# Kernel optimization log

Hardware: AMD Instinct MI355X
Metric: run time of the kernel (lower is better)

## Reference

```python
import jax, jax.numpy as jnp
import numpy as np

N_HEAD = 16
N_KV_HEAD = 8
HEAD_DIM = 128
N_EMBED = 2048
EPS = 1.1920929e-07  # torch default eps for fp32 rms_norm


def _apply_rotary_emb(x, cos, sin):
    # x: (B, T, H, D); cos/sin: (1, T, 1, D//2)  (nanochat-style half rotation)
    d = x.shape[-1] // 2
    x1, x2 = x[..., :d], x[..., d:]
    y1 = x1 * cos + x2 * sin
    y2 = -x1 * sin + x2 * cos
    return jnp.concatenate([y1, y2], axis=-1).astype(x.dtype)


def _rms_norm(x):
    return x * jax.lax.rsqrt(jnp.mean(jnp.square(x), axis=-1, keepdims=True) + EPS)


def setup_inputs() -> dict:
    key = jax.random.key(0)
    ks = jax.random.split(key, 5)
    B, T = 2, 2048
    kv_dim = N_KV_HEAD * HEAD_DIM
    x = jax.random.normal(ks[0], (B, T, N_EMBED), dtype=jnp.float32)
    w_attn = jax.random.normal(ks[1], (N_EMBED + 2 * kv_dim, N_EMBED), dtype=jnp.float32) * 0.02
    w_proj = jax.random.normal(ks[2], (N_EMBED, N_EMBED), dtype=jnp.float32) * 0.02
    # realistic RoPE tables
    half = HEAD_DIM // 2
    inv_freq = 1.0 / (10000.0 ** (jnp.arange(half, dtype=jnp.float32) / half))
    freqs = jnp.arange(T, dtype=jnp.float32)[:, None] * inv_freq[None, :]  # (T, half)
    cos = jnp.cos(freqs)[None, :, None, :]
    sin = jnp.sin(freqs)[None, :, None, :]
    return {"x": x, "w_attn": w_attn, "w_proj": w_proj, "cos": cos, "sin": sin}


def reference(x, w_attn, w_proj, cos, sin):
    B, T, C = x.shape
    kv_dim = N_KV_HEAD * HEAD_DIM
    qkv = jnp.einsum('btc,oc->bto', x, w_attn)  # (B, T, C + 2*kv_dim)
    q = qkv[..., :C].reshape(B, T, N_HEAD, HEAD_DIM)
    k = qkv[..., C:C + kv_dim].reshape(B, T, N_KV_HEAD, HEAD_DIM)
    v = qkv[..., C + kv_dim:].reshape(B, T, N_KV_HEAD, HEAD_DIM)
    q = _rms_norm(_apply_rotary_emb(q, cos, sin))
    k = _rms_norm(_apply_rotary_emb(k, cos, sin))
    # GQA: repeat kv heads to match query heads
    rep = N_HEAD // N_KV_HEAD
    k = jnp.repeat(k, rep, axis=2)  # (B, T, n_head, D)
    v = jnp.repeat(v, rep, axis=2)
    scale = 1.0 / jnp.sqrt(jnp.float32(HEAD_DIM))
    scores = jnp.einsum('bqhd,bkhd->bhqk', q, k) * scale  # (B, H, T, T)
    causal = jnp.tril(jnp.ones((T, T), dtype=bool))
    scores = jnp.where(causal[None, None], scores, jnp.finfo(scores.dtype).min)
    attn = jax.nn.softmax(scores, axis=-1)
    y = jnp.einsum('bhqk,bkhd->bqhd', attn, v).reshape(B, T, C)
    return jnp.einsum('btc,oc->bto', y, w_proj)
```

## Files before the change

### kernel.cpp

```cpp
#include <hip/hip_runtime.h>

#define B_ 2
#define T_ 2048
#define NH 16
#define NKV 8
#define HD 128
#define C_ 2048
#define KVD (NKV*HD)
#define QKVD (C_ + 2*KVD)
#define NTOK (B_*T_)

typedef __bf16 bf16_t;
typedef __bf16 bf16x2_t __attribute__((ext_vector_type(2)));
typedef __bf16 bf16x4_t __attribute__((ext_vector_type(4)));
typedef __bf16 bf16x8_t __attribute__((ext_vector_type(8)));
typedef float f32x4_t __attribute__((ext_vector_type(4)));
typedef float f32x16_t __attribute__((ext_vector_type(16)));
typedef int i32x4_t __attribute__((ext_vector_type(4)));

__device__ __forceinline__ f32x4_t mfma16(bf16x8_t a, bf16x8_t b, f32x4_t c) {
  return __builtin_amdgcn_mfma_f32_16x16x32_bf16(a, b, c, 0, 0, 0);
}
__device__ __forceinline__ f32x16_t mfma32(bf16x8_t a, bf16x8_t b, f32x16_t c) {
  return __builtin_amdgcn_mfma_f32_32x32x16_bf16(a, b, c, 0, 0, 0);
}
__device__ __forceinline__ f32x16_t zero16() {
  f32x16_t z;
  #pragma unroll
  for (int i = 0; i < 16; i++) z[i] = 0.f;
  return z;
}
__device__ __forceinline__ int pk2(float a, float b) {
  bf16x2_t t; t[0] = (bf16_t)a; t[1] = (bf16_t)b;
  return __builtin_bit_cast(int, t);
}

#define GLDS16(gp, lp) __builtin_amdgcn_global_load_lds( \
    (const __attribute__((address_space(1))) void*)(gp), \
    (__attribute__((address_space(3))) void*)(lp), 16, 0, 0)

#define CFENCE() asm volatile("" ::: "memory")

#define KSTR 132
#define VSTR 68

__global__ __launch_bounds__(256) void cvt3_kernel(const float* __restrict__ s0, bf16_t* __restrict__ d0,
                                                   const float* __restrict__ s1, bf16_t* __restrict__ d1,
                                                   const float* __restrict__ s2, bf16_t* __restrict__ d2) {
  int bid = blockIdx.x;
  const float* s; bf16_t* d; int off;
  if (bid < 8192)       { s = s0; d = d0; off = bid; }
  else if (bid < 16384) { s = s1; d = d1; off = bid - 8192; }
  else                  { s = s2; d = d2; off = bid - 16384; }
  int i = (off * 256 + threadIdx.x) * 4;
  const float4 v = *(const float4*)(s + i);
  bf16x4_t o;
  o[0] = (bf16_t)v.x; o[1] = (bf16_t)v.y; o[2] = (bf16_t)v.z; o[3] = (bf16_t)v.w;
  *(bf16x4_t*)(d + i) = o;
}

__global__ __launch_bounds__(512, 1) void gemm8p(const bf16_t* __restrict__ A,
                                                 const bf16_t* __restrict__ Bm,
                                                 bf16_t* __restrict__ Cb,
                                                 int M, int N, int K) {
  __shared__ __align__(16) bf16_t As[2][256 * 64];
  __shared__ __align__(16) bf16_t Bs[2][256 * 64];
  int tid = threadIdx.x;
  int wave = tid >> 6, lane = tid & 63;
  int quad = lane >> 4, l16 = lane & 15;
  int wm = wave >> 2, wn = wave & 3;
  int gx = gridDim.x, nwg = gx * gridDim.y;
  int flat = blockIdx.y * gx + blockIdx.x;
  int swz = (flat & 7) * (nwg >> 3) + (flat >> 3);
  int bm = (swz / gx) * 256, bn = (swz % gx) * 256;
  int scol = ((tid & 7) ^ ((tid >> 3) & 7)) * 8;
  int srow = tid >> 3;
  const bf16_t* pa = A + (size_t)(bm + srow) * K + scol;
  const bf16_t* pb = Bm + (size_t)(bn + srow) * K + scol;

#define STAGE_A8(buf, tile, h) { \
    GLDS16(pa + (size_t)((h)*128 + 0) * K + (size_t)(tile)*64, &As[buf][((h)*128 + 0 + wave*8)*64]); \
    GLDS16(pa + (size_t)((h)*128 + 64) * K + (size_t)(tile)*64, &As[buf][((h)*128 + 64 + wave*8)*64]); }
#define STAGE_B8(buf, tile, h) { \
    GLDS16(pb + (size_t)((h)*128 + 0) * K + (size_t)(tile)*64, &Bs[buf][((h)*128 + 0 + wave*8)*64]); \
    GLDS16(pb + (size_t)((h)*128 + 64) * K + (size_t)(tile)*64, &Bs[buf][((h)*128 + 64 + wave*8)*64]); }

  f32x4_t acc[8][4];
  #pragma unroll
  for (int i = 0; i < 8; i++)
    #pragma unroll
    for (int j = 0; j < 4; j++) acc[i][j] = (f32x4_t){0.f, 0.f, 0.f, 0.f};

  int nt = K >> 6;
  STAGE_A8(0, 0, 0); STAGE_A8(0, 0, 1); STAGE_B8(0, 0, 0); STAGE_B8(0, 0, 1);
  STAGE_B8(1, 1, 0); STAGE_B8(1, 1, 1);
  asm volatile("s_waitcnt vmcnt(4)" ::: "memory");
  CFENCE(); __builtin_amdgcn_s_barrier(); CFENCE();

  for (int s = 0; s < nt; ++s) {
    int b = s & 1;
    bf16x8_t bfr[4][2];
    #pragma unroll
    for (int jph = 0; jph < 4; ++jph) {
      const int kh = jph >> 1;
      const int mg = jph & 1;
      if (mg == 0) {
        #pragma unroll
        for (int ni = 0; ni < 4; ni++)
          bfr[ni][kh] = *(const bf16x8_t*)&Bs[b][(wn*64 + ni*16 + l16)*64 + (((kh*4 + quad) ^ (l16 & 7))*8)];
      }
      bf16x8_t af[4];
      #pragma unroll
      for (int i = 0; i < 4; i++)
        af[i] = *(const bf16x8_t*)&As[b][(wm*128 + (mg*4 + i)*16 + l16)*64 + (((kh*4 + quad) ^ (l16 & 7))*8)];
      if (jph == 0) { if (s + 1 < nt) STAGE_A8(1 - b, s + 1, 0); }
      if (jph == 1) { if (s + 1 < nt) STAGE_A8(1 - b, s + 1, 1); }
      if (jph == 3) {
        if (s + 2 < nt) {
          STAGE_B8(b, s + 2, 0);
          STAGE_B8(b, s + 2, 1);
          asm volatile("s_waitcnt vmcnt(4)" ::: "memory");
        } else {
          asm volatile("s_waitcnt vmcnt(0)" ::: "memory");
        }
      }
      CFENCE(); __builtin_amdgcn_s_barrier(); CFENCE();
      __builtin_amdgcn_s_setprio(1);
      #pragma unroll
      for (int i = 0; i < 4; i++)
        #pragma unroll
        for (int ni = 0; ni < 4; ni++)
          acc[mg*4 + i][ni] = mfma16(af[i], bfr[ni][kh], acc[mg*4 + i][ni]);
      __builtin_amdgcn_s_setprio(0);
      CFENCE(); __builtin_amdgcn_s_barrier(); CFENCE();
    }
  }
  #pragma unroll
  for (int mi = 0; mi < 8; mi++)
    #pragma unroll
    for (int ni = 0; ni < 4; ni++) {
      int row0 = bm + wm*128 + mi*16 + quad*4;
      int col  = bn + wn*64 + ni*16 + l16;
      #pragma unroll
      for (int r = 0; r < 4; r++)
        Cb[(size_t)(row0 + r) * N + col] = (bf16_t)acc[mi][ni][r];
    }
#undef STAGE_A8
#undef STAGE_B8
}

template<int BM>
__global__ __launch_bounds__(512, 1) void gemm_nt2(const bf16_t* __restrict__ A,
                                                   const bf16_t* __restrict__ Bm,
                                                   float* __restrict__ Cf, bf16_t* __restrict__ Cb,
                                                   int M, int N, int K) {
  constexpr int MR = BM / 32;
  constexpr int RA = BM / 64;
  __shared__ __align__(16) bf16_t As[2][BM * 64];
  __shared__ __align__(16) bf16_t Bs[2][256 * 64];
  int tid = threadIdx.x;
  int wave = tid >> 6, lane = tid & 63;
  int quad = lane >> 4, l16 = lane & 15;
  int wm = wave >> 2, wn = wave & 3;
  int gx = gridDim.x;
  int nwg = gx * gridDim.y;
  int flat = blockIdx.y * gx + blockIdx.x;
  int swz = (flat & 7) * (nwg >> 3) + (flat >> 3);
  int bm = (swz / gx) * BM, bn = (swz % gx) * 256;
  int scol = (((tid & 7) ^ ((tid >> 3) & 7))) * 8;
  const bf16_t* pa = A + (size_t)(bm + (tid >> 3)) * K + scol;
  const bf16_t* pb = Bm + (size_t)(bn + (tid >> 3)) * K + scol;

  f32x4_t acc[MR][4];
  #pragma unroll
  for (int i = 0; i < MR; i++)
    #pragma unroll
    for (int j = 0; j < 4; j++) acc[i][j] = (f32x4_t){0.f, 0.f, 0.f, 0.f};

  int nt = K >> 6;
  #pragma unroll
  for (int r = 0; r < RA; r++) GLDS16(pa + (size_t)(r * 64) * K, &As[0][(r * 64 + wave * 8) * 64]);
  #pragma unroll
  for (int r = 0; r < 4; r++)  GLDS16(pb + (size_t)(r * 64) * K, &Bs[0][(r * 64 + wave * 8) * 64]);
  __syncthreads();

  for (int t = 0; t < nt; t++) {
    int cur = t & 1;
    if (t + 1 < nt) {
      int k1 = (t + 1) * 64;
      #pragma unroll
      for (int r = 0; r < RA; r++) GLDS16(pa + (size_t)(r * 64) * K + k1, &As[1 - cur][(r * 64 + wave * 8) * 64]);
      #pragma unroll
      for (int r = 0; r < 4; r++)  GLDS16(pb + (size_t)(r * 64) * K + k1, &Bs[1 - cur][(r * 64 + wave * 8) * 64]);
    }
    bf16x8_t bfr[4][2];
    #pragma unroll
    for (int ni = 0; ni < 4; ni++)
      #pragma unroll
      for (int kh = 0; kh < 2; kh++) {
        int blk = (kh * 4 + quad) ^ (l16 & 7);
        bfr[ni][kh] = *(const bf16x8_t*)&Bs[cur][(wn * 64 + ni * 16 + l16) * 64 + blk * 8];
      }
    #pragma unroll
    for (int g = 0; g < MR / 2; g++) {
      bf16x8_t af[2][2];
      #pragma unroll
      for (int i = 0; i < 2; i++)
        #pragma unroll
        for (int kh = 0; kh < 2; kh++) {
          int blk = (kh * 4 + quad) ^ (l16 & 7);
          af[i][kh] = *(const bf16x8_t*)&As[cur][(wm * (BM / 2) + (g * 2 + i) * 16 + l16) * 64 + blk * 8];
        }
      #pragma unroll
      for (int kh = 0; kh < 2; kh++)
        #pragma unroll
        for (int i = 0; i < 2; i++)
          #pragma unroll
          for (int ni = 0; ni < 4; ni++)
            acc[g * 2 + i][ni] = mfma16(af[i][kh], bfr[ni][kh], acc[g * 2 + i][ni]);
    }
    __syncthreads();
  }
  #pragma unroll
  for (int mi = 0; mi < MR; mi++)
    #pragma unroll
    for (int ni = 0; ni < 4; ni++) {
      int row0 = bm + wm * (BM / 2) + mi * 16 + quad * 4;
      int col  = bn + wn * 64 + ni * 16 + l16;
      if (Cb) {
        #pragma unroll
        for (int r = 0; r < 4; r++)
          Cb[(size_t)(row0 + r) * N + col] = (bf16_t)acc[mi][ni][r];
      } else {
        #pragma unroll
        for (int r = 0; r < 4; r++)
          Cf[(size_t)(row0 + r) * N + col] = acc[mi][ni][r];
      }
    }
}

__global__ __launch_bounds__(256) void rope_tv_kernel(const bf16_t* __restrict__ qkv,
    const float* __restrict__ cosb, const float* __restrict__ sinb,
    bf16_t* __restrict__ qb, bf16_t* __restrict__ kb, bf16_t* __restrict__ vt) {
  __shared__ bf16_t TT[64*136];
  int bid = blockIdx.x;
  int tid = threadIdx.x;
  if (bid < 24576) {
    int token = bid & 4095;
    int slot = (bid >> 12) * 4 + (tid >> 6);
    int lane = tid & 63;
    int b = token >> 11, s = token & 2047;
    const bf16_t* row = qkv + (size_t)token * QKVD;
    int base_in = (slot < 16) ? slot * HD : C_ + (slot - 16) * HD;
    float x1 = (float)row[base_in + lane];
    float x2 = (float)row[base_in + 64 + lane];
    float c = cosb[s*64 + lane], sn = sinb[s*64 + lane];
    float y1 = x1*c + x2*sn;
    float y2 = x2*c - x1*sn;
    float ss = y1*y1 + y2*y2;
    ss += __shfl_xor(ss, 1);  ss += __shfl_xor(ss, 2);  ss += __shfl_xor(ss, 4);
    ss += __shfl_xor(ss, 8);  ss += __shfl_xor(ss, 16); ss += __shfl_xor(ss, 32);
    float r = rsqrtf(ss * (1.0f/128.0f) + 1.1920929e-07f);
    bf16_t* dst;
    if (slot < 16) {
      r *= 0.08838834764831845f * 1.4426950408889634f;
      dst = qb + ((size_t)(b*NH + slot) * T_ + s) * HD;
    } else {
      dst = kb + ((size_t)(b*NKV + (slot-16)) * T_ + s) * HD;
    }
    dst[lane]      = (bf16_t)(y1 * r);
    dst[lane + 64] = (bf16_t)(y2 * r);
  } else {
    int id = bid - 24576;
    int bk = id & 15;
    int s0 = (id >> 4) * 64;
    int b = bk >> 3, kv = bk & 7;
    int row = tid >> 2, c0 = (tid & 3) * 32;
    const bf16_t* src = qkv + (size_t)(b*T_ + s0 + row) * QKVD + C_ + KVD + kv*HD + c0;
    #pragma unroll
    for (int s4 = 0; s4 < 4; s4++)
      *(bf16x8_t*)&TT[row*136 + c0 + s4*8] = *(const bf16x8_t*)(src + s4*8);
    __syncthreads();
    #pragma unroll
    for (int s2 = 0; s2 < 2; s2++) {
      int d = (tid >> 2) + s2*64;
      #pragma unroll
      for (int s = 0; s < 2; s++) {
        int g = (tid & 3) * 8 + s*32;
        bf16x8_t pk;
        #pragma unroll
        for (int e = 0; e < 8; e++) pk[e] = TT[(g + e)*136 + d];
        *(bf16x8_t*)(vt + ((size_t)bk * HD + d) * T_ + s0 + g) = pk;
      }
    }
  }
}

__global__ __launch_bounds__(512, 1) void attn_kernel(const bf16_t* __restrict__ qb,
    const bf16_t* __restrict__ kb, const bf16_t* __restrict__ vt, bf16_t* __restrict__ yb) {
  __shared__ __align__(16) bf16_t Ks[2][2][64*KSTR];
  __shared__ __align__(16) bf16_t Vs[2][2][128*VSTR];
  int L = blockIdx.x;
  int bh = L & 31;
  int qt = 15 - (L >> 5);
  int b = bh >> 4, h = bh & 15, kvh = h >> 1;
  int tid = threadIdx.x;
  int wv = tid >> 6;
  int g  = wv >> 2;
  int sq = wv & 3;
  int lane = tid & 63;
  int l32 = lane & 31, half = lane >> 5;
  int t256 = tid & 255;
  const bf16_t* Qp = qb + (size_t)bh * T_ * HD;
  const bf16_t* Kp = kb + (size_t)(b*NKV + kvh) * T_ * HD;
  const bf16_t* Vt = vt + (size_t)(b*NKV + kvh) * HD * T_;

  int krow = t256 >> 2, kcb = (t256 & 3) * 32;
  int vd = t256 >> 1,  vcb = (t256 & 1) * 32;

  int h0 = qt + 1;
  int kt0 = g * h0;

  int qrow = qt*128 + sq*32 + l32;
  bf16x8_t qf[8];
  #pragma unroll
  for (int kc = 0; kc < 8; kc++)
    qf[kc] = *(const bf16x8_t*)(Qp + (size_t)qrow * HD + kc*16 + half*8);

  float mrow = -1e30f, lrow = 0.f;
  f32x16_t o[4];
  #pragma unroll
  for (int mb = 0; mb < 4; mb++) o[mb] = zero16();

  bf16x8_t kreg[4], vreg[4];
  {
    const bf16_t* srck = Kp + (size_t)(kt0*64 + krow) * HD + kcb;
    const bf16_t* srcv = Vt + (size_t)vd * T_ + kt0*64 + vcb;
    #pragma unroll
    for (int s2 = 0; s2 < 4; s2++) { kreg[s2] = *(const bf16x8_t*)(srck + s2*8);
                                     vreg[s2] = *(const bf16x8_t*)(srcv + s2*8); }
  }
  #pragma unroll
  for (int s2 = 0; s2 < 4; s2++) { *(bf16x8_t*)&Ks[g][0][krow*KSTR + kcb + s2*8] = kreg[s2];
                                   *(bf16x8_t*)&Vs[g][0][vd*VSTR  + vcb + s2*8] = vreg[s2]; }

  for (int t = 0; t < h0; t++) {
    __syncthreads();
    int cur = t & 1;
    if (t + 1 < h0) {
      int k1 = (kt0 + t + 1) * 64;
      const bf16_t* srck = Kp + (size_t)(k1 + krow) * HD + kcb;
      const bf16_t* srcv = Vt + (size_t)vd * T_ + k1 + vcb;
      #pragma unroll
      for (int s2 = 0; s2 < 4; s2++) { kreg[s2] = *(const bf16x8_t*)(srck + s2*8);
                                       vreg[s2] = *(const bf16x8_t*)(srcv + s2*8); }
    }
    int k0 = (kt0 + t) * 64;
    f32x16_t sacc[2];
    sacc[0] = zero16(); sacc[1] = zero16();
    #pragma unroll
    for (int kc = 0; kc < 8; kc++)
      #pragma unroll
      for (int mb = 0; mb < 2; mb++) {
        bf16x8_t kf = *(const bf16x8_t*)&Ks[g][cur][(mb*32 + l32)*KSTR + kc*16 + half*8];
        sacc[mb] = mfma32(kf, qf[kc], sacc[mb]);
      }
    if (k0 + 63 > qt*128 + sq*32) {
      #pragma unroll
      for (int mb = 0; mb < 2; mb++)
        #pragma unroll
        for (int r = 0; r < 16; r++) {
          int key = k0 + mb*32 + (r&3) + 8*(r>>2) + 4*half;
          if (key > qrow) sacc[mb][r] = -1e30f;
        }
    }
    float tm[16];
    #pragma unroll
    for (int r = 0; r < 16; r++) tm[r] = fmaxf(sacc[0][r], sacc[1][r]);
    #pragma unroll
    for (int st = 8; st >= 1; st >>= 1)
      #pragma unroll
      for (int r = 0; r < st; r++) tm[r] = fmaxf(tm[r], tm[r + st]);
    float mx = fmaxf(tm[0], __shfl_xor(tm[0], 32));
    if (!__all(mx - mrow <= 8.0f)) {
      float mnew = fmaxf(mrow, mx);
      float alpha = exp2f(mrow - mnew);
      mrow = mnew;
      lrow *= alpha;
      #pragma unroll
      for (int mb = 0; mb < 4; mb++) o[mb] = o[mb] * alpha;
    }
    #pragma unroll
    for (int mb = 0; mb < 2; mb++)
      #pragma unroll
      for (int r = 0; r < 16; r++) sacc[mb][r] = exp2f(sacc[mb][r] - mrow);
    float ts[16];
    #pragma unroll
    for (int r = 0; r < 16; r++) ts[r] = sacc[0][r] + sacc[1][r];
    #pragma unroll
    for (int st = 8; st >= 1; st >>= 1)
      #pragma unroll
      for (int r = 0; r < st; r++) ts[r] += ts[r + st];
    lrow += ts[0] + __shfl_xor(ts[0], 32);
    int P2[2][4][2];
    #pragma unroll
    for (int mb = 0; mb < 2; mb++)
      #pragma unroll
      for (int gg = 0; gg < 4; gg++) {
        P2[mb][gg][0] = pk2(sacc[mb][4*gg+0], sacc[mb][4*gg+1]);
        P2[mb][gg][1] = pk2(sacc[mb][4*gg+2], sacc[mb][4*gg+3]);
      }
    #pragma unroll
    for (int kc = 0; kc < 4; kc++) {
      int mb = kc >> 1, c = kc & 1;
      int o0 = half ? P2[mb][2*c+1][0] : P2[mb][2*c][0];
      int o1 = half ? P2[mb][2*c+1][1] : P2[mb][2*c][1];
      int s0 = half ? P2[mb][2*c][0]   : P2[mb][2*c+1][0];
      int s1 = half ? P2[mb][2*c][1]   : P2[mb][2*c+1][1];
      int r0 = __shfl_xor(s0, 32);
      int r1 = __shfl_xor(s1, 32);
      i32x4_t wvv;
      wvv[0] = half ? r0 : o0;
      wvv[1] = half ? r1 : o1;
      wvv[2] = half ? o0 : r0;
      wvv[3] = half ? o1 : r1;
      bf16x8_t pf = __builtin_bit_cast(bf16x8_t, wvv);
      #pragma unroll
      for (int mbd = 0; mbd < 4; mbd++) {
        bf16x8_t vf = *(const bf16x8_t*)&Vs[g][cur][(mbd*32 + l32)*VSTR + kc*16 + half*8];
        o[mbd] = mfma32(vf, pf, o[mbd]);
      }
    }
    if (t + 1 < h0) {
      #pragma unroll
      for (int s2 = 0; s2 < 4; s2++) { *(bf16x8_t*)&Ks[g][1-cur][krow*KSTR + kcb + s2*8] = kreg[s2];
                                       *(bf16x8_t*)&Vs[g][1-cur][vd*VSTR  + vcb + s2*8] = vreg[s2]; }
    }
  }
  __syncthreads();
  float* MG = (float*)Vs;
  int mbase = (sq*64 + lane) * 66;
  if (g == 1) {
    #pragma unroll
    for (int mb = 0; mb < 4; mb++)
      #pragma unroll
      for (int r = 0; r < 16; r++) MG[mbase + mb*16 + r] = o[mb][r];
    MG[mbase + 64] = mrow;
    MG[mbase + 65] = lrow;
  }
  __syncthreads();
  if (g == 0) {
    float m1 = MG[mbase + 64], l1v = MG[mbase + 65];
    float mm = fmaxf(mrow, m1);
    float a0 = exp2f(mrow - mm), a1 = exp2f(m1 - mm);
    float invl = 1.0f / (lrow * a0 + l1v * a1);
    a0 *= invl; a1 *= invl;
    bf16_t* OL = &((bf16_t*)Ks)[sq * (32 * KSTR)];
    #pragma unroll
    for (int mb = 0; mb < 4; mb++)
      #pragma unroll
      for (int rr = 0; rr < 4; rr++) {
        bf16x4_t pk;
        #pragma unroll
        for (int jj = 0; jj < 4; jj++)
          pk[jj] = (bf16_t)(o[mb][rr*4+jj] * a0 + MG[mbase + mb*16 + rr*4 + jj] * a1);
        *(bf16x4_t*)&OL[l32*KSTR + mb*32 + rr*8 + half*4] = pk;
      }
    int tok = qt*128 + sq*32 + l32;
    bf16_t* dst = yb + ((size_t)(b*T_ + tok) * NH + h) * HD + half*64;
    #pragma unroll
    for (int jj = 0; jj < 8; jj++)
      *(bf16x8_t*)(dst + jj*8) = *(const bf16x8_t*)&OL[l32*KSTR + half*64 + jj*8];
  }
}

extern "C" void kernel_launch(void* const* d_in, const int* in_sizes, int n_in,
                              void* d_out, int out_size, void* d_ws, size_t ws_size,
                              hipStream_t stream) {
  const float* x      = (const float*)d_in[0];
  const float* w_attn = (const float*)d_in[1];
  const float* w_proj = (const float*)d_in[2];
  const float* cosb   = (const float*)d_in[3];
  const float* sinb   = (const float*)d_in[4];
  float* out = (float*)d_out;

  bf16_t* xb   = (bf16_t*)d_ws;
  bf16_t* wab  = xb + 8388608;
  bf16_t* wpb  = wab + 8388608;
  bf16_t* qkvb = wpb + 4194304;
  bf16_t* qb   = qkvb + 16777216;
  bf16_t* kb   = qb + 8388608;
  bf16_t* vt   = kb + 4194304;
  bf16_t* yb   = vt + 4194304;

  cvt3_kernel<<<20480, 256, 0, stream>>>(x, xb, w_attn, wab, w_proj, wpb);

  gemm8p<<<dim3(16, 16), 512, 0, stream>>>(xb, wab, qkvb, NTOK, QKVD, C_);

  rope_tv_kernel<<<25088, 256, 0, stream>>>(qkvb, cosb, sinb, qb, kb, vt);

  attn_kernel<<<512, 512, 0, stream>>>(qb, kb, vt, yb);

  gemm_nt2<128><<<dim3(8, 32), 512, 0, stream>>>(yb, wpb, out, nullptr, NTOK, C_, C_);
}
```

Measured before the change: 315.1 us.

## Skew softmax/PV against QK^T across wave groups with triple-buffered V

Wave group 1 now runs the softmax and PV step of the previous key tile before the QK^T of the current tile, while group 0 keeps the original order. Group 1's V tiles go into a 3-slot ring in shared memory so the delayed PV can still read its tile. The aim is to interleave MFMA-heavy and exp/VALU-heavy phases across the two groups sharing a CU, so matrix and vector units are busy at the same time. The cost is extra LDS for the V ring, more code from the macro bodies, and more register pressure from keeping scores live across iterations.

```diff
diff --git a/kernel.cpp b/kernel.cpp
--- a/kernel.cpp
+++ b/kernel.cpp
@@ -299,7 +299,7 @@
 __global__ __launch_bounds__(512, 1) void attn_kernel(const bf16_t* __restrict__ qb,
     const bf16_t* __restrict__ kb, const bf16_t* __restrict__ vt, bf16_t* __restrict__ yb) {
   __shared__ __align__(16) bf16_t Ks[2][2][64*KSTR];
-  __shared__ __align__(16) bf16_t Vs[2][2][128*VSTR];
+  __shared__ __align__(16) bf16_t Vall[5][128*VSTR];
   int L = blockIdx.x;
   int bh = L & 31;
   int qt = 15 - (L >> 5);
@@ -331,6 +331,93 @@
   f32x16_t o[4];
   #pragma unroll
   for (int mb = 0; mb < 4; mb++) o[mb] = zero16();
+  f32x16_t sv[2];
+
+#define QKT_BODY(KBASE) { \
+    sv[0] = zero16(); sv[1] = zero16(); \
+    _Pragma("unroll") \
+    for (int kc = 0; kc < 8; kc++) { \
+      _Pragma("unroll") \
+      for (int mb = 0; mb < 2; mb++) { \
+        bf16x8_t kf = *(const bf16x8_t*)&(KBASE)[(mb*32 + l32)*KSTR + kc*16 + half*8]; \
+        sv[mb] = mfma32(kf, qf[kc], sv[mb]); \
+      } \
+    } \
+  }
+#define MASK_BODY(K0V) { \
+    if ((K0V) + 63 > qt*128 + sq*32) { \
+      _Pragma("unroll") \
+      for (int mb = 0; mb < 2; mb++) { \
+        _Pragma("unroll") \
+        for (int r = 0; r < 16; r++) { \
+          int key = (K0V) + mb*32 + (r&3) + 8*(r>>2) + 4*half; \
+          if (key > qrow) sv[mb][r] = -1e30f; \
+        } \
+      } \
+    } \
+  }
+#define SMPV_BODY(VBASE) { \
+    float tm[16]; \
+    _Pragma("unroll") \
+    for (int r = 0; r < 16; r++) tm[r] = fmaxf(sv[0][r], sv[1][r]); \
+    _Pragma("unroll") \
+    for (int st = 8; st >= 1; st >>= 1) { \
+      _Pragma("unroll") \
+      for (int r = 0; r < st; r++) tm[r] = fmaxf(tm[r], tm[r + st]); \
+    } \
+    float mx = fmaxf(tm[0], __shfl_xor(tm[0], 32)); \
+    if (!__all(mx - mrow <= 8.0f)) { \
+      float mnew = fmaxf(mrow, mx); \
+      float alpha = exp2f(mrow - mnew); \
+      mrow = mnew; lrow *= alpha; \
+      _Pragma("unroll") \
+      for (int mb = 0; mb < 4; mb++) o[mb] = o[mb] * alpha; \
+    } \
+    _Pragma("unroll") \
+    for (int mb = 0; mb < 2; mb++) { \
+      _Pragma("unroll") \
+      for (int r = 0; r < 16; r++) sv[mb][r] = exp2f(sv[mb][r] - mrow); \
+    } \
+    float tsum[16]; \
+    _Pragma("unroll") \
+    for (int r = 0; r < 16; r++) tsum[r] = sv[0][r] + sv[1][r]; \
+    _Pragma("unroll") \
+    for (int st = 8; st >= 1; st >>= 1) { \
+      _Pragma("unroll") \
+      for (int r = 0; r < st; r++) tsum[r] += tsum[r + st]; \
+    } \
+    lrow += tsum[0] + __shfl_xor(tsum[0], 32); \
+    int P2[2][4][2]; \
+    _Pragma("unroll") \
+    for (int mb = 0; mb < 2; mb++) { \
+      _Pragma("unroll") \
+      for (int gg = 0; gg < 4; gg++) { \
+        P2[mb][gg][0] = pk2(sv[mb][4*gg+0], sv[mb][4*gg+1]); \
+        P2[mb][gg][1] = pk2(sv[mb][4*gg+2], sv[mb][4*gg+3]); \
+      } \
+    } \
+    _Pragma("unroll") \
+    for (int kc = 0; kc < 4; kc++) { \
+      int mbq = kc >> 1, c = kc & 1; \
+      int o0 = half ? P2[mbq][2*c+1][0] : P2[mbq][2*c][0]; \
+      int o1 = half ? P2[mbq][2*c+1][1] : P2[mbq][2*c][1]; \
+      int s0 = half ? P2[mbq][2*c][0]   : P2[mbq][2*c+1][0]; \
+      int s1 = half ? P2[mbq][2*c][1]   : P2[mbq][2*c+1][1]; \
+      int r0 = __shfl_xor(s0, 32); \
+      int r1 = __shfl_xor(s1, 32); \
+      i32x4_t wvv; \
+      wvv[0] = half ? r0 : o0; \
+      wvv[1] = half ? r1 : o1; \
+      wvv[2] = half ? o0 : r0; \
+      wvv[3] = half ? o1 : r1; \
+      bf16x8_t pf = __builtin_bit_cast(bf16x8_t, wvv); \
+      _Pragma("unroll") \
+      for (int mbd = 0; mbd < 4; mbd++) { \
+        bf16x8_t vf = *(const bf16x8_t*)&(VBASE)[(mbd*32 + l32)*VSTR + kc*16 + half*8]; \
+        o[mbd] = mfma32(vf, pf, o[mbd]); \
+      } \
+    } \
+  }
 
   bf16x8_t kreg[4], vreg[4];
   {
@@ -340,13 +427,19 @@
     for (int s2 = 0; s2 < 4; s2++) { kreg[s2] = *(const bf16x8_t*)(srck + s2*8);
                                      vreg[s2] = *(const bf16x8_t*)(srcv + s2*8); }
   }
-  #pragma unroll
-  for (int s2 = 0; s2 < 4; s2++) { *(bf16x8_t*)&Ks[g][0][krow*KSTR + kcb + s2*8] = kreg[s2];
-                                   *(bf16x8_t*)&Vs[g][0][vd*VSTR  + vcb + s2*8] = vreg[s2]; }
-
+  {
+    bf16_t* v0 = (g == 0) ? Vall[0] : Vall[2];
+    #pragma unroll
+    for (int s2 = 0; s2 < 4; s2++) { *(bf16x8_t*)&Ks[g][0][krow*KSTR + kcb + s2*8] = kreg[s2];
+                                     *(bf16x8_t*)&v0[vd*VSTR + vcb + s2*8] = vreg[s2]; }
+  }
+
+  int vq = 0;
   for (int t = 0; t < h0; t++) {
     __syncthreads();
     int cur = t & 1;
+    int vqn = (vq == 2) ? 0 : vq + 1;
+    int vqp = (vq == 0) ? 2 : vq - 1;
     if (t + 1 < h0) {
       int k1 = (kt0 + t + 1) * 64;
       const bf16_t* srck = Kp + (size_t)(k1 + krow) * HD + kcb;
@@ -356,89 +449,29 @@
                                        vreg[s2] = *(const bf16x8_t*)(srcv + s2*8); }
     }
     int k0 = (kt0 + t) * 64;
-    f32x16_t sacc[2];
-    sacc[0] = zero16(); sacc[1] = zero16();
-    #pragma unroll
-    for (int kc = 0; kc < 8; kc++)
-      #pragma unroll
-      for (int mb = 0; mb < 2; mb++) {
-        bf16x8_t kf = *(const bf16x8_t*)&Ks[g][cur][(mb*32 + l32)*KSTR + kc*16 + half*8];
-        sacc[mb] = mfma32(kf, qf[kc], sacc[mb]);
-      }
-    if (k0 + 63 > qt*128 + sq*32) {
-      #pragma unroll
-      for (int mb = 0; mb < 2; mb++)
-        #pragma unroll
-        for (int r = 0; r < 16; r++) {
-          int key = k0 + mb*32 + (r&3) + 8*(r>>2) + 4*half;
-          if (key > qrow) sacc[mb][r] = -1e30f;
-        }
-    }
-    float tm[16];
-    #pragma unroll
-    for (int r = 0; r < 16; r++) tm[r] = fmaxf(sacc[0][r], sacc[1][r]);
-    #pragma unroll
-    for (int st = 8; st >= 1; st >>= 1)
-      #pragma unroll
-      for (int r = 0; r < st; r++) tm[r] = fmaxf(tm[r], tm[r + st]);
-    float mx = fmaxf(tm[0], __shfl_xor(tm[0], 32));
-    if (!__all(mx - mrow <= 8.0f)) {
-      float mnew = fmaxf(mrow, mx);
-      float alpha = exp2f(mrow - mnew);
-      mrow = mnew;
-      lrow *= alpha;
-      #pragma unroll
-      for (int mb = 0; mb < 4; mb++) o[mb] = o[mb] * alpha;
-    }
-    #pragma unroll
-    for (int mb = 0; mb < 2; mb++)
-      #pragma unroll
-      for (int r = 0; r < 16; r++) sacc[mb][r] = exp2f(sacc[mb][r] - mrow);
-    float ts[16];
-    #pragma unroll
-    for (int r = 0; r < 16; r++) ts[r] = sacc[0][r] + sacc[1][r];
-    #pragma unroll
-    for (int st = 8; st >= 1; st >>= 1)
-      #pragma unroll
-      for (int r = 0; r < st; r++) ts[r] += ts[r + st];
-    lrow += ts[0] + __shfl_xor(ts[0], 32);
-    int P2[2][4][2];
-    #pragma unroll
-    for (int mb = 0; mb < 2; mb++)
-      #pragma unroll
-      for (int gg = 0; gg < 4; gg++) {
-        P2[mb][gg][0] = pk2(sacc[mb][4*gg+0], sacc[mb][4*gg+1]);
-        P2[mb][gg][1] = pk2(sacc[mb][4*gg+2], sacc[mb][4*gg+3]);
-      }
-    #pragma unroll
-    for (int kc = 0; kc < 4; kc++) {
-      int mb = kc >> 1, c = kc & 1;
-      int o0 = half ? P2[mb][2*c+1][0] : P2[mb][2*c][0];
-      int o1 = half ? P2[mb][2*c+1][1] : P2[mb][2*c][1];
-      int s0 = half ? P2[mb][2*c][0]   : P2[mb][2*c+1][0];
-      int s1 = half ? P2[mb][2*c][1]   : P2[mb][2*c+1][1];
-      int r0 = __shfl_xor(s0, 32);
-      int r1 = __shfl_xor(s1, 32);
-      i32x4_t wvv;
-      wvv[0] = half ? r0 : o0;
-      wvv[1] = half ? r1 : o1;
-      wvv[2] = half ? o0 : r0;
-      wvv[3] = half ? o1 : r1;
-      bf16x8_t pf = __builtin_bit_cast(bf16x8_t, wvv);
-      #pragma unroll
-      for (int mbd = 0; mbd < 4; mbd++) {
-        bf16x8_t vf = *(const bf16x8_t*)&Vs[g][cur][(mbd*32 + l32)*VSTR + kc*16 + half*8];
-        o[mbd] = mfma32(vf, pf, o[mbd]);
-      }
+    if (g == 0) {
+      QKT_BODY(Ks[0][cur]);
+      MASK_BODY(k0);
+      SMPV_BODY(Vall[cur]);
+    } else {
+      if (t > 0) { SMPV_BODY(Vall[2 + vqp]); }
+      QKT_BODY(Ks[1][cur]);
+      MASK_BODY(k0);
     }
     if (t + 1 < h0) {
+      bf16_t* vw = (g == 0) ? Vall[1 - cur] : Vall[2 + vqn];
       #pragma unroll
       for (int s2 = 0; s2 < 4; s2++) { *(bf16x8_t*)&Ks[g][1-cur][krow*KSTR + kcb + s2*8] = kreg[s2];
-                                       *(bf16x8_t*)&Vs[g][1-cur][vd*VSTR  + vcb + s2*8] = vreg[s2]; }
-    }
+                                       *(bf16x8_t*)&vw[vd*VSTR + vcb + s2*8] = vreg[s2]; }
+    }
+    vq = vqn;
+  }
+  if (g == 1) {
+    int vqp2 = (vq == 0) ? 2 : vq - 1;
+    SMPV_BODY(Vall[2 + vqp2]);
   }
   __syncthreads();
-  float* MG = (float*)Vs;
+  float* MG = (float*)Vall;
   int mbase = (sq*64 + lane) * 66;
   if (g == 1) {
     #pragma unroll
@@ -472,6 +505,9 @@
     for (int jj = 0; jj < 8; jj++)
       *(bf16x8_t*)(dst + jj*8) = *(const bf16x8_t*)&OL[l32*KSTR + half*64 + jj*8];
   }
+#undef QKT_BODY
+#undef MASK_BODY
+#undef SMPV_BODY
 }
 
 extern "C" void kernel_launch(void* const* d_in, const int* in_sizes, int n_in,
```

New measurement: 329.2 us. 4.5% more time.
